# Performance work log

Hardware: AMD Instinct MI355X
Metric: run time of the kernel (lower is better)

Reference implementation:

```python
import jax, jax.numpy as jnp
import numpy as np

SINKHORN_ALPHA = 20.0
WEIGHT_LOSS_ECR = 100.0
OT_MAX_ITER = 100
STOP_THR = 0.005
EPS = 1e-16


def setup_inputs() -> dict:
    key = jax.random.key(0)
    # cost matrix: topics x vocab, nonnegative
    M = jax.random.uniform(key, (2000, 20000), dtype=jnp.float32)
    return {"M": M}


def reference(M):
    n, m = M.shape
    a = jnp.full((n, 1), 1.0 / n, dtype=M.dtype)  # uniform row marginal
    b = jnp.full((m, 1), 1.0 / m, dtype=M.dtype)  # uniform col marginal
    K = jnp.exp(-M * SINKHORN_ALPHA)              # Gibbs kernel, (n, m)

    u0 = jnp.full((n, 1), 1.0 / n, dtype=M.dtype)
    v0 = jnp.zeros((m, 1), dtype=M.dtype)
    err0 = jnp.asarray(1.0, dtype=M.dtype)
    cpt0 = jnp.asarray(0, dtype=jnp.int32)

    def cond(carry):
        u, v, err, cpt = carry
        return (err > STOP_THR) & (cpt < OT_MAX_ITER)

    def body(carry):
        u, v, err, cpt = carry
        v = b / (K.T @ u + EPS)          # (m, 1)
        u = a / (K @ v + EPS)            # (n, 1)
        cpt = cpt + 1
        # convergence check every 50 iterations (cpt % 50 == 1), as in torch
        bb = v * (K.T @ u)               # (m, 1) implied col marginal
        err_new = jnp.max(jnp.sum(jnp.abs(bb - b), axis=0))
        err = jnp.where(cpt % 50 == 1, err_new.astype(err.dtype), err)
        return (u, v, err, cpt)

    u, v, err, cpt = jax.lax.while_loop(cond, body, (u0, v0, err0, cpt0))

    transp = u * (K * v.T)               # transport plan, (n, m)
    loss_ECR = jnp.sum(transp * M)
    return loss_ECR * WEIGHT_LOSS_ECR
```

## Files before the change

### kernel.cpp

```cpp
#include <hip/hip_runtime.h>

typedef unsigned int uint32;
typedef unsigned long long uint64;
typedef float floatx2 __attribute__((ext_vector_type(2)));

#define ROWS_R 2000
#define COLS_R 20000
#define NBLK   256
#define NTHR   1024
#define NWAVE  16
#define CPB    80
#define CSTR   501
#define KDW    (CPB*CSTR)
#define KGUARD 16
#define USLOTS 101

static constexpr float A_MARG = 1.0f / 2000.0f;
static constexpr float B_MARG = 1.0f / 20000.0f;
static constexpr float EPSV   = 1e-16f;
static constexpr float THR    = 0.005f;
static constexpr float NALPHA = -20.0f;

__device__ __forceinline__ void st_dev_f32(float* p, float v) {
    __hip_atomic_store(p, v, __ATOMIC_RELAXED, __HIP_MEMORY_SCOPE_AGENT);
}
__device__ __forceinline__ float ld_dev_f32(const float* p) {
    return __hip_atomic_load(const_cast<float*>(p), __ATOMIC_RELAXED, __HIP_MEMORY_SCOPE_AGENT);
}
__device__ __forceinline__ void st_dev_f32x2(float* p, float x, float y) {
    union { float2 f; uint64 q; } u; u.f = make_float2(x, y);
    __hip_atomic_store(reinterpret_cast<uint64*>(p), u.q, __ATOMIC_RELAXED, __HIP_MEMORY_SCOPE_AGENT);
}
__device__ __forceinline__ float2 ld_dev_f32x2(const float* p) {
    union { float2 f; uint64 q; } u;
    u.q = __hip_atomic_load(reinterpret_cast<uint64*>(const_cast<float*>(p)),
                            __ATOMIC_RELAXED, __HIP_MEMORY_SCOPE_AGENT);
    return u.f;
}


__device__ __forceinline__ float halfpair_sum(float x) {
#if __has_builtin(__builtin_amdgcn_permlane32_swap)
    int xi = __float_as_int(x);
    auto sw = __builtin_amdgcn_permlane32_swap(xi, xi, false, false);
    return __int_as_float(sw[0]) + __int_as_float(sw[1]);
#else
    return x + __shfl_xor(x, 32, 64);
#endif
}

__device__ __forceinline__ float pair16_sum(float x) {
#if __has_builtin(__builtin_amdgcn_permlane16_swap)
    int xi = __float_as_int(x);
    auto sw = __builtin_amdgcn_permlane16_swap(xi, xi, false, false);
    return __int_as_float(sw[0]) + __int_as_float(sw[1]);
#else
    return x + __shfl_xor(x, 16, 64);
#endif
}

template <int CTRL>
__device__ __forceinline__ float dpp_ror_add(float x) {
#if __has_builtin(__builtin_amdgcn_update_dpp)
    int xi = __float_as_int(x);
    int sh = __builtin_amdgcn_update_dpp(0, xi, CTRL, 0xF, 0xF, true);
    return x + __int_as_float(sh);
#else
    const int off = (CTRL == 0x128) ? 8 : (CTRL == 0x124) ? 4 : (CTRL == 0x122) ? 2 : 1;
    return x + __shfl_xor(x, off, 64);
#endif
}

__device__ __forceinline__ float rowsum16(float x) {
    x = dpp_ror_add<0x128>(x);
    x = dpp_ror_add<0x124>(x);
    x = dpp_ror_add<0x122>(x);
    x = dpp_ror_add<0x121>(x);
    return x;
}

__device__ __forceinline__ void grid_barrier(uint32* ctrl, uint32 rnd) {
    asm volatile("s_waitcnt vmcnt(0)" ::: "memory");
    __syncthreads();
    if (threadIdx.x == 0) {
        const int gid = (int)(blockIdx.x >> 5);
        uint32* gcnt = ctrl + 128 + gid * 64;
        uint32* ggen = ctrl + 768 + gid * 64;
        uint32 a = __hip_atomic_fetch_add(gcnt, 1u, __ATOMIC_RELAXED, __HIP_MEMORY_SCOPE_AGENT);
        if (a == rnd * 32u + 31u) {
            uint32 r = __hip_atomic_fetch_add(ctrl, 1u, __ATOMIC_RELAXED, __HIP_MEMORY_SCOPE_AGENT);
            if (r == rnd * 8u + 7u) {
#pragma unroll
                for (int g = 0; g < 8; ++g)
                    __hip_atomic_store(ctrl + 768 + g * 64, rnd + 1u,
                                       __ATOMIC_RELAXED, __HIP_MEMORY_SCOPE_AGENT);
            }
        }
        while (__hip_atomic_load(ggen, __ATOMIC_RELAXED, __HIP_MEMORY_SCOPE_AGENT) < rnd + 1u)
            __builtin_amdgcn_s_sleep(1);
    }
    __syncthreads();
}

__global__ __launch_bounds__(256) void init_kernel(float* __restrict__ u_rot,
                                                   uint32* __restrict__ ctrl,
                                                   float* __restrict__ err2,
                                                   float* __restrict__ loss) {
    int idx = blockIdx.x * 256 + threadIdx.x;
    if (idx < 1280) ctrl[idx] = 0u;
    if (idx == 0) { err2[0] = 0.f; err2[1] = 0.f; *loss = 0.f; }
    if (idx < 2048) u_rot[idx] = (idx < ROWS_R) ? A_MARG : 0.0f;
}

__global__ __launch_bounds__(NTHR, 1) void sinkhorn_lds(
    const float* __restrict__ M,
    float* __restrict__ u_rot,
    float* __restrict__ P2,
    uint32* __restrict__ ctrl,
    float* __restrict__ err2,
    float* __restrict__ loss,
    float* __restrict__ out) {
    __shared__ uint32 sK[KDW + KGUARD];
    __shared__ float  s_vloc[CPB];
    __shared__ float  s_vprev[CPB];
    __shared__ float  s_red[NWAVE * 8];
    __shared__ int    s_flag;

    const int tid  = threadIdx.x;
    const int lane = tid & 63;
    const int wav  = tid >> 6;
    const int b    = blockIdx.x;
    const int j0   = b * CPB;
    uint32 bar = 0;

    for (int i = tid; i < KDW + KGUARD; i += NTHR) sK[i] = 0u;
    __syncthreads();
    for (int q = wav; q < 500; q += NWAVE) {
#pragma unroll
        for (int ph = 0; ph < 2; ++ph) {
            const int cl = ph * 64 + lane;
            const int j  = j0 + cl;
            if ((ph == 0 || lane < 16) && j < COLS_R) {
                const float* mp = M + (size_t)(4 * q) * COLS_R + j;
                float k0 = __expf(NALPHA * mp[0]);
                float k1 = __expf(NALPHA * mp[COLS_R]);
                float k2 = __expf(NALPHA * mp[2 * COLS_R]);
                float k3 = __expf(NALPHA * mp[3 * COLS_R]);
                int lo = __builtin_amdgcn_cvt_pk_fp8_f32(k0, k1, 0, false);
                int hi = __builtin_amdgcn_cvt_pk_fp8_f32(k2, k3, lo, true);
                sK[cl * CSTR + q] = (uint32)hi;
            }
        }
    }
    __syncthreads();

    int usel = 0;

    for (int t = 1; t <= 100; ++t) {
        const bool chk  = (t == 2) || (t == 52);
        const int  slot = (t == 52) ? 1 : 0;

        const float4* u4 = reinterpret_cast<const float4*>(u_rot + (size_t)usel * 2048);
        float4 u_r[8];
#pragma unroll
        for (int s = 0; s < 8; ++s) u_r[s] = u4[s * 64 + lane];

        float e = 0.f;
#pragma unroll
        for (int q = 0; q < 5; ++q) {
            const int jl = wav * 5 + q;
            float acc = 0.f;
#pragma unroll
            for (int s = 0; s < 8; ++s) {
                uint32 kw = sK[jl * CSTR + s * 64 + lane];
                floatx2 f01 = __builtin_amdgcn_cvt_pk_f32_fp8(kw, false);
                floatx2 f23 = __builtin_amdgcn_cvt_pk_f32_fp8(kw, true);
                acc += f01.x * u_r[s].x + f01.y * u_r[s].y + f23.x * u_r[s].z + f23.y * u_r[s].w;
            }
            acc = halfpair_sum(acc);
            acc = pair16_sum(acc);
            acc = rowsum16(acc);
            if (lane == 0) {
                float vnew = B_MARG / (acc + EPSV);
                if (chk) {
                    float vold = s_vloc[jl];
                    s_vprev[jl] = vold;
                    if (j0 + jl < COLS_R) e += fabsf(vold * acc - B_MARG);
                }
                s_vloc[jl] = vnew;
            }
        }
        if (chk && lane == 0) s_red[wav] = e;
        __syncthreads();

        {
            const int rg = lane >> 4;
            const int rm = lane & 15;
            const int qb = wav * 32 + 2 * rm;
            float4 pb0 = make_float4(0.f, 0.f, 0.f, 0.f);
            float4 pb1 = make_float4(0.f, 0.f, 0.f, 0.f);
#pragma unroll 5
            for (int jp = 0; jp < 20; ++jp) {
                const int cl = jp * 4 + rg;
                uint32 ka = sK[cl * CSTR + qb];
                uint32 kb = sK[cl * CSTR + qb + 1];
                float  vv = s_vloc[cl];
                floatx2 a01 = __builtin_amdgcn_cvt_pk_f32_fp8(ka, false);
                floatx2 a23 = __builtin_amdgcn_cvt_pk_f32_fp8(ka, true);
                floatx2 b01 = __builtin_amdgcn_cvt_pk_f32_fp8(kb, false);
                floatx2 b23 = __builtin_amdgcn_cvt_pk_f32_fp8(kb, true);
                pb0.x += a01.x * vv; pb0.y += a01.y * vv;
                pb0.z += a23.x * vv; pb0.w += a23.y * vv;
                pb1.x += b01.x * vv; pb1.y += b01.y * vv;
                pb1.z += b23.x * vv; pb1.w += b23.y * vv;
            }
            pb0.x = pair16_sum(pb0.x);  pb0.y = pair16_sum(pb0.y);
            pb0.z = pair16_sum(pb0.z);  pb0.w = pair16_sum(pb0.w);
            pb1.x = pair16_sum(pb1.x);  pb1.y = pair16_sum(pb1.y);
            pb1.z = pair16_sum(pb1.z);  pb1.w = pair16_sum(pb1.w);
            pb0.x = halfpair_sum(pb0.x);  pb0.y = halfpair_sum(pb0.y);
            pb0.z = halfpair_sum(pb0.z);  pb0.w = halfpair_sum(pb0.w);
            pb1.x = halfpair_sum(pb1.x);  pb1.y = halfpair_sum(pb1.y);
            pb1.z = halfpair_sum(pb1.z);  pb1.w = halfpair_sum(pb1.w);
            if (lane < 16) {
                float* dst = P2 + (size_t)(wav * 16 + lane) * 2048 + b * 8;
                st_dev_f32x2(dst,     pb0.x, pb0.y);
                st_dev_f32x2(dst + 2, pb0.z, pb0.w);
                st_dev_f32x2(dst + 4, pb1.x, pb1.y);
                st_dev_f32x2(dst + 6, pb1.z, pb1.w);
            }
        }

        if (chk && tid == 0) {
            float s = 0.f;
            for (int k = 0; k < NWAVE; ++k) s += s_red[k];
            if (s != 0.f) atomicAdd(&err2[slot], s);
        }
        grid_barrier(ctrl, bar++);

        if (chk) {
            if (tid == 0) s_flag = (ld_dev_f32(&err2[slot]) <= THR) ? 1 : 0;
            __syncthreads();
            if (s_flag) {
                if (tid < CPB) s_vloc[tid] = s_vprev[tid];
                __syncthreads();
                break;
            }
        }

        {
            float2 pr = ld_dev_f32x2(P2 + (size_t)b * 2048 + tid * 2);
            pr.x = dpp_ror_add<0x124>(pr.x);  pr.y = dpp_ror_add<0x124>(pr.y);
            pr.x = dpp_ror_add<0x128>(pr.x);  pr.y = dpp_ror_add<0x128>(pr.y);
            pr.x = pair16_sum(pr.x);          pr.y = pair16_sum(pr.y);
            pr.x = halfpair_sum(pr.x);        pr.y = halfpair_sum(pr.y);
            if (lane < 4) {
                s_red[wav * 8 + 2 * lane]     = pr.x;
                s_red[wav * 8 + 2 * lane + 1] = pr.y;
            }
        }
        __syncthreads();
        if (tid < 8) {
            float s = 0.f;
            for (int w = 0; w < NWAVE; ++w) s += s_red[w * 8 + tid];
            const int row = 8 * b + tid;
            float val = (row < ROWS_R) ? A_MARG / (s + EPSV) : 0.0f;
            st_dev_f32(u_rot + (size_t)t * 2048 + row, val);
        }
        usel = t;
        grid_barrier(ctrl, bar++);
    }

    {
        const float* uf = u_rot + (size_t)usel * 2048;
        float acc = 0.f;
        for (int r = wav; r < ROWS_R; r += NWAVE) {
            const float uu = uf[r];
            const float* mp = M + (size_t)r * COLS_R + j0;
#pragma unroll
            for (int ph = 0; ph < 2; ++ph) {
                const int cl = ph * 64 + lane;
                if ((ph == 0 || lane < 16) && (j0 + cl) < COLS_R) {
                    float m = mp[cl];
                    acc += uu * __expf(NALPHA * m) * s_vloc[cl] * m;
                }
            }
        }
        acc = halfpair_sum(acc);
        acc = pair16_sum(acc);
        acc = rowsum16(acc);
        if (lane == 0) s_red[wav] = acc;
        __syncthreads();
        if (tid == 0) {
            float s = 0.f;
            for (int k = 0; k < NWAVE; ++k) s += s_red[k];
            if (s != 0.f) atomicAdd(loss, s);
        }
    }
    grid_barrier(ctrl, bar++);
    if (b == 0 && tid == 0) out[0] = ld_dev_f32(loss) * 100.0f;
}


__device__ __forceinline__ float block_reduce_sum256(float v) {
#pragma unroll
    for (int o = 32; o; o >>= 1) v += __shfl_down(v, o, 64);
    __shared__ float smem[4];
    int lane = threadIdx.x & 63, w = threadIdx.x >> 6;
    if (lane == 0) smem[w] = v;
    __syncthreads();
    v = (threadIdx.x < 4) ? smem[threadIdx.x] : 0.0f;
    v += __shfl_down(v, 2, 64);
    v += __shfl_down(v, 1, 64);
    return v;
}

__global__ __launch_bounds__(256) void fb_init(float* u, float* vden, int* done, float* err, float* loss) {
    int idx = blockIdx.x * 256 + threadIdx.x;
    if (idx == 0) { *done = 0; *err = 0.0f; *loss = 0.0f; }
    if (idx < ROWS_R) u[idx] = A_MARG;
    if (idx < COLS_R) vden[idx] = 0.0f;
}
__global__ __launch_bounds__(256) void fb_colpass(const float* __restrict__ M, const float* __restrict__ u,
                                                  float* __restrict__ vden, const int* __restrict__ done) {
    if (*done) return;
    int c4 = blockIdx.x * 256 + threadIdx.x;
    if (c4 >= 5000) return;
    int r0 = blockIdx.y * 50;
    float4 acc = make_float4(0.f, 0.f, 0.f, 0.f);
    for (int r = r0; r < r0 + 50; ++r) {
        float ui = u[r];
        float4 mm = reinterpret_cast<const float4*>(M)[(size_t)r * 5000 + c4];
        acc.x += __expf(NALPHA * mm.x) * ui; acc.y += __expf(NALPHA * mm.y) * ui;
        acc.z += __expf(NALPHA * mm.z) * ui; acc.w += __expf(NALPHA * mm.w) * ui;
    }
    atomicAdd(&vden[c4 * 4 + 0], acc.x); atomicAdd(&vden[c4 * 4 + 1], acc.y);
    atomicAdd(&vden[c4 * 4 + 2], acc.z); atomicAdd(&vden[c4 * 4 + 3], acc.w);
}
__global__ __launch_bounds__(256) void fb_finv(float* v, float* vden, const int* done) {
    if (*done) return;
    int j = blockIdx.x * 256 + threadIdx.x;
    if (j < COLS_R) { v[j] = B_MARG / (vden[j] + EPSV); vden[j] = 0.0f; }
}
__global__ __launch_bounds__(256) void fb_rowpass(const float* __restrict__ M, const float* __restrict__ v,
                                                  float* __restrict__ u, const int* __restrict__ done) {
    if (*done) return;
    int row = blockIdx.x;
    const float4* v4 = reinterpret_cast<const float4*>(v);
    float acc = 0.0f;
    for (int c4 = threadIdx.x; c4 < 5000; c4 += 256) {
        float4 mm = reinterpret_cast<const float4*>(M)[(size_t)row * 5000 + c4];
        float4 vv = v4[c4];
        acc += __expf(NALPHA * mm.x) * vv.x + __expf(NALPHA * mm.y) * vv.y
             + __expf(NALPHA * mm.z) * vv.z + __expf(NALPHA * mm.w) * vv.w;
    }
    float s = block_reduce_sum256(acc);
    if (threadIdx.x == 0) u[row] = A_MARG / (s + EPSV);
}
__global__ __launch_bounds__(256) void fb_errfin(const float* v, float* vden, float* err, const int* done) {
    if (*done) return;
    int j = blockIdx.x * 256 + threadIdx.x;
    float local = 0.0f;
    if (j < COLS_R) { local = fabsf(v[j] * vden[j] - B_MARG); vden[j] = 0.0f; }
    float s = block_reduce_sum256(local);
    if (threadIdx.x == 0) atomicAdd(err, s);
}
__global__ void fb_check(int* done, float* err) {
    if (threadIdx.x == 0) { if (!*done && *err <= THR) *done = 1; *err = 0.0f; }
}
__global__ __launch_bounds__(256) void fb_loss(const float* __restrict__ M, const float* __restrict__ u,
                                               const float* __restrict__ v, float* __restrict__ loss) {
    int row = blockIdx.x;
    const float4* M4p = reinterpret_cast<const float4*>(M + (size_t)row * COLS_R);
    const float4* v4 = reinterpret_cast<const float4*>(v);
    float acc = 0.0f;
    for (int c4 = threadIdx.x; c4 < 5000; c4 += 256) {
        float4 mm = M4p[c4]; float4 vv = v4[c4];
        acc += __expf(NALPHA * mm.x) * vv.x * mm.x + __expf(NALPHA * mm.y) * vv.y * mm.y
             + __expf(NALPHA * mm.z) * vv.z * mm.z + __expf(NALPHA * mm.w) * vv.w * mm.w;
    }
    float s = block_reduce_sum256(acc);
    if (threadIdx.x == 0) atomicAdd(loss, s * u[row]);
}
__global__ void fb_writeout(float* out, const float* loss) {
    if (threadIdx.x == 0) out[0] = *loss * 100.0f;
}


extern "C" void kernel_launch(void* const* d_in, const int* in_sizes, int n_in,
                              void* d_out, int out_size, void* d_ws, size_t ws_size,
                              hipStream_t stream) {
    const float* M = (const float*)d_in[0];
    char* base = (char*)d_ws;

    const size_t OFF_CTRL = 0;
    const size_t OFF_ERR  = 8192;
    const size_t OFF_LOSS = 8320;
    const size_t OFF_UROT = 8448;
    const size_t OFF_P    = OFF_UROT + (size_t)USLOTS * 2048 * 4;
    const size_t NEED     = OFF_P + (size_t)NBLK * 2048 * 4;

    if (ws_size >= NEED) {
        uint32* ctrl  = (uint32*)(base + OFF_CTRL);
        float*  err2  = (float*)(base + OFF_ERR);
        float*  loss  = (float*)(base + OFF_LOSS);
        float*  u_rot = (float*)(base + OFF_UROT);
        float*  P2    = (float*)(base + OFF_P);

        init_kernel<<<8, 256, 0, stream>>>(u_rot, ctrl, err2, loss);
        sinkhorn_lds<<<NBLK, NTHR, 0, stream>>>(M, u_rot, P2, ctrl, err2, loss, (float*)d_out);
    } else {
        int*   done = (int*)(base + 0);
        float* err  = (float*)(base + 8);
        float* loss = (float*)(base + 16);
        float* u    = (float*)(base + 64);
        float* v    = (float*)(base + 64 + 8192);
        float* vden = (float*)(base + 64 + 8192 + 80000);

        fb_init<<<79, 256, 0, stream>>>(u, vden, done, err, loss);
        dim3 cgrid(20, 40);
        for (int t = 1; t <= 100; ++t) {
            fb_colpass<<<cgrid, 256, 0, stream>>>(M, u, vden, done);
            fb_finv<<<79, 256, 0, stream>>>(v, vden, done);
            fb_rowpass<<<ROWS_R, 256, 0, stream>>>(M, v, u, done);
            if (t == 1 || t == 51) {
                fb_colpass<<<cgrid, 256, 0, stream>>>(M, u, vden, done);
                fb_errfin<<<79, 256, 0, stream>>>(v, vden, err, done);
                fb_check<<<1, 64, 0, stream>>>(done, err);
            }
        }
        fb_loss<<<ROWS_R, 256, 0, stream>>>(M, u, v, loss);
        fb_writeout<<<1, 64, 0, stream>>>((float*)d_out, loss);
    }
}
```

Measured before the change: 334.1 us.

## Replace per-iteration second grid barrier with per-block u-ready flags

Each block now publishes a per-block iteration flag after writing its slice of u, instead of joining a second grid-wide barrier at the end of every Sinkhorn iteration. At the start of the next iteration, 256 threads each poll one producer's flag until it reaches t-1. A final wait before the loss pass covers the no-break case. The aim is to cut the atomic counter traffic and the serialised barrier latency of one of the two grid syncs per iteration. In exchange, correctness now depends on the flag ordering (vmcnt wait before the relaxed flag store) and on every block polling 256 flags.

Measured after the change: 354.5 us. +6.1%, slower.

```diff
diff --git a/kernel.cpp b/kernel.cpp
--- a/kernel.cpp
+++ b/kernel.cpp
@@ -27,6 +27,12 @@
 __device__ __forceinline__ float ld_dev_f32(const float* p) {
     return __hip_atomic_load(const_cast<float*>(p), __ATOMIC_RELAXED, __HIP_MEMORY_SCOPE_AGENT);
 }
+__device__ __forceinline__ void st_dev_u32(uint32* p, uint32 v) {
+    __hip_atomic_store(p, v, __ATOMIC_RELAXED, __HIP_MEMORY_SCOPE_AGENT);
+}
+__device__ __forceinline__ uint32 ld_dev_u32(const uint32* p) {
+    return __hip_atomic_load(const_cast<uint32*>(p), __ATOMIC_RELAXED, __HIP_MEMORY_SCOPE_AGENT);
+}
 __device__ __forceinline__ void st_dev_f32x2(float* p, float x, float y) {
     union { float2 f; uint64 q; } u; u.f = make_float2(x, y);
     __hip_atomic_store(reinterpret_cast<uint64*>(p), u.q, __ATOMIC_RELAXED, __HIP_MEMORY_SCOPE_AGENT);
@@ -104,10 +110,12 @@
 
 __global__ __launch_bounds__(256) void init_kernel(float* __restrict__ u_rot,
                                                    uint32* __restrict__ ctrl,
+                                                   uint32* __restrict__ uflag,
                                                    float* __restrict__ err2,
                                                    float* __restrict__ loss) {
     int idx = blockIdx.x * 256 + threadIdx.x;
     if (idx < 1280) ctrl[idx] = 0u;
+    if (idx < 1024) uflag[idx] = 0u;
     if (idx == 0) { err2[0] = 0.f; err2[1] = 0.f; *loss = 0.f; }
     if (idx < 2048) u_rot[idx] = (idx < ROWS_R) ? A_MARG : 0.0f;
 }
@@ -117,6 +125,7 @@
     float* __restrict__ u_rot,
     float* __restrict__ P2,
     uint32* __restrict__ ctrl,
+    uint32* __restrict__ uflag,
     float* __restrict__ err2,
     float* __restrict__ loss,
     float* __restrict__ out) {
@@ -155,10 +164,19 @@
     __syncthreads();
 
     int usel = 0;
+    int broke = 0;
 
     for (int t = 1; t <= 100; ++t) {
         const bool chk  = (t == 2) || (t == 52);
         const int  slot = (t == 52) ? 1 : 0;
+
+        if (t > 1) {
+            if (tid < 256) {
+                uint32* f = &uflag[tid * 4];
+                while (ld_dev_u32(f) < (uint32)(t - 1)) __builtin_amdgcn_s_sleep(1);
+            }
+            __syncthreads();
+        }
 
         const float4* u4 = reinterpret_cast<const float4*>(u_rot + (size_t)usel * 2048);
         float4 u_r[8];
@@ -244,6 +262,7 @@
             if (s_flag) {
                 if (tid < CPB) s_vloc[tid] = s_vprev[tid];
                 __syncthreads();
+                broke = 1;
                 break;
             }
         }
@@ -267,9 +286,20 @@
             float val = (row < ROWS_R) ? A_MARG / (s + EPSV) : 0.0f;
             st_dev_f32(u_rot + (size_t)t * 2048 + row, val);
         }
+        if (wav == 0) {
+            asm volatile("s_waitcnt vmcnt(0)" ::: "memory");
+            if (lane == 0) st_dev_u32(&uflag[b * 4], (uint32)t);
+        }
         usel = t;
-        grid_barrier(ctrl, bar++);
-    }
+    }
+
+    if (!broke) {
+        if (tid < 256) {
+            uint32* f = &uflag[tid * 4];
+            while (ld_dev_u32(f) < 100u) __builtin_amdgcn_s_sleep(1);
+        }
+    }
+    __syncthreads();
 
     {
         const float* uf = u_rot + (size_t)usel * 2048;
@@ -393,22 +423,24 @@
     const float* M = (const float*)d_in[0];
     char* base = (char*)d_ws;
 
-    const size_t OFF_CTRL = 0;
-    const size_t OFF_ERR  = 8192;
-    const size_t OFF_LOSS = 8320;
-    const size_t OFF_UROT = 8448;
-    const size_t OFF_P    = OFF_UROT + (size_t)USLOTS * 2048 * 4;
-    const size_t NEED     = OFF_P + (size_t)NBLK * 2048 * 4;
+    const size_t OFF_CTRL  = 0;
+    const size_t OFF_UFLAG = 8192;
+    const size_t OFF_ERR   = 8192 + 4096;
+    const size_t OFF_LOSS  = OFF_ERR + 128;
+    const size_t OFF_UROT  = OFF_LOSS + 128;
+    const size_t OFF_P     = OFF_UROT + (size_t)USLOTS * 2048 * 4;
+    const size_t NEED      = OFF_P + (size_t)NBLK * 2048 * 4;
 
     if (ws_size >= NEED) {
         uint32* ctrl  = (uint32*)(base + OFF_CTRL);
+        uint32* uflag = (uint32*)(base + OFF_UFLAG);
         float*  err2  = (float*)(base + OFF_ERR);
         float*  loss  = (float*)(base + OFF_LOSS);
         float*  u_rot = (float*)(base + OFF_UROT);
         float*  P2    = (float*)(base + OFF_P);
 
-        init_kernel<<<8, 256, 0, stream>>>(u_rot, ctrl, err2, loss);
-        sinkhorn_lds<<<NBLK, NTHR, 0, stream>>>(M, u_rot, P2, ctrl, err2, loss, (float*)d_out);
+        init_kernel<<<8, 256, 0, stream>>>(u_rot, ctrl, uflag, err2, loss);
+        sinkhorn_lds<<<NBLK, NTHR, 0, stream>>>(M, u_rot, P2, ctrl, uflag, err2, loss, (float*)d_out);
     } else {
         int*   done = (int*)(base + 0);
         float* err  = (float*)(base + 8);
```
